# Optimization experiments

Measured on AMD Instinct MI355X. Metric: run time of the kernel, lower is better.

The kernel has to match this reference:

```python
import jax, jax.numpy as jnp
import numpy as np
from jax import lax

CLASSES = 6
R = 8            # zoom_factor
FEAT = 32        # DUC loops i,j in range(32)
OUT_PAD = 304    # DUC hardcodes zeros(b,6,304,304)
IMG = 256        # original image H=W -> final bilinear resize target
BN_EPS = 1e-5
DN = ('NCHW', 'OIHW', 'NCHW')


def _duc(x):
    # x: [B, classes*r*r, H', W'] ; original loop only reads top-left 32x32
    x = x[:, :, :FEAT, :FEAT]
    B = x.shape[0]
    # channel order in original: view(b, classes, r*r) -> (classes, r, r)
    y = x.reshape(B, CLASSES, R, R, FEAT, FEAT)
    y = y.transpose(0, 1, 4, 2, 5, 3).reshape(B, CLASSES, FEAT * R, FEAT * R)  # [B,6,256,256]
    pad = OUT_PAD - FEAT * R
    return jnp.pad(y, ((0, 0), (0, 0), (0, pad), (0, pad)))  # zeros ring like torch.zeros buffer


def _bilinear_align_corners(x, oh, ow):
    b, c, h, w = x.shape
    ys = jnp.linspace(0.0, h - 1.0, oh)
    xs = jnp.linspace(0.0, w - 1.0, ow)
    y0 = jnp.floor(ys).astype(jnp.int32)
    x0 = jnp.floor(xs).astype(jnp.int32)
    y1 = jnp.minimum(y0 + 1, h - 1)
    x1 = jnp.minimum(x0 + 1, w - 1)
    wy = (ys - y0)[None, None, :, None]
    wx = (xs - x0)[None, None, None, :]
    rows = x[:, :, y0, :] * (1.0 - wy) + x[:, :, y1, :] * wy          # [b,c,oh,w]
    out = rows[:, :, :, x0] * (1.0 - wx) + rows[:, :, :, x1] * wx     # [b,c,oh,ow]
    return out


def setup_inputs() -> dict:
    key = jax.random.key(0)
    ks = jax.random.split(key, 8)
    x = jax.random.normal(ks[0], (16, 5632, 32, 32), jnp.float32)
    w1 = jax.random.normal(ks[1], (512, 5632, 1, 1), jnp.float32) * 0.02
    gamma = 1.0 + 0.1 * jax.random.normal(ks[2], (512,), jnp.float32)
    beta = 0.1 * jax.random.normal(ks[3], (512,), jnp.float32)
    mean = 0.1 * jax.random.normal(ks[4], (512,), jnp.float32)
    var = jax.random.uniform(ks[5], (512,), jnp.float32, 0.5, 1.5)
    w2 = jax.random.normal(ks[6], (CLASSES * R * R, 512, 1, 1), jnp.float32) * 0.02
    b2 = jax.random.normal(ks[7], (CLASSES * R * R,), jnp.float32) * 0.02
    return {'x': x, 'w1': w1, 'gamma': gamma, 'beta': beta, 'mean': mean, 'var': var, 'w2': w2, 'b2': b2}


def reference(x, w1, gamma, beta, mean, var, w2, b2):
    # cls head: 1x1 conv with padding=1 (quirk in source) -> 34x34 map
    h = lax.conv_general_dilated(x, w1, (1, 1), ((1, 1), (1, 1)), dimension_numbers=DN)
    inv = lax.rsqrt(var + BN_EPS)
    h = (h - mean[None, :, None, None]) * (inv * gamma)[None, :, None, None] + beta[None, :, None, None]
    h = jax.nn.relu(h)  # Dropout2d is identity at inference
    h = lax.conv_general_dilated(h, w2, (1, 1), ((0, 0), (0, 0)), dimension_numbers=DN)
    h = h + b2[None, :, None, None]            # [B,384,34,34]
    h = _duc(h)                                # [B,6,304,304]
    h = jax.nn.softmax(h, axis=1)
    return _bilinear_align_corners(h, IMG, IMG)  # [B,6,256,256]
```

## Files before the change

### kernel.cpp

```cpp
#include <hip/hip_runtime.h>
#include <hip/hip_bf16.h>
#include <stdint.h>

typedef float f32x4 __attribute__((ext_vector_type(4)));
typedef short s16x8 __attribute__((ext_vector_type(8)));
typedef unsigned short u16;

__device__ __forceinline__ u16 f2bf(float f) {
  uint32_t u = __float_as_uint(f);
  u = (u + 0x7fffu + ((u >> 16) & 1u)) >> 16;
  return (u16)u;
}

__device__ __forceinline__ u16 cvt_bf(float f) {
  union { __hip_bfloat16 h; u16 u; } c;
  c.h = __float2bfloat16(f);
  return c.u;
}

__device__ __forceinline__ void wg_barrier_lds() {
  __builtin_amdgcn_sched_barrier(0);
  asm volatile("s_waitcnt lgkmcnt(0)" ::: "memory");
  __builtin_amdgcn_s_barrier();
  __builtin_amdgcn_sched_barrier(0);
}

__global__ void k_params(const float* __restrict__ gamma, const float* __restrict__ beta,
                         const float* __restrict__ mean, const float* __restrict__ var,
                         float* __restrict__ bnS, float* __restrict__ bnT) {
  int i = threadIdx.x;
  if (i < 512) {
    float s = gamma[i] * rsqrtf(var[i] + 1e-5f);
    bnS[i] = s;
    bnT[i] = beta[i] - mean[i] * s;
  }
}

__global__ void k_convert(const float* __restrict__ in, u16* __restrict__ out, int n4) {
  int i = blockIdx.x * blockDim.x + threadIdx.x;
  if (i < n4) {
    float4 v = ((const float4*)in)[i];
    ushort4 o;
    o.x = f2bf(v.x); o.y = f2bf(v.y); o.z = f2bf(v.z); o.w = f2bf(v.w);
    ((ushort4*)out)[i] = o;
  }
}

__global__ void k_border2(const float* __restrict__ w2, const float* __restrict__ b2,
                          const float* __restrict__ bnT, float* __restrict__ border2) {
  int o = blockIdx.x;
  int l = threadIdx.x;
  float s = 0.f;
  for (int j = 0; j < 8; ++j) {
    int c = l + 64 * j;
    s += w2[o * 512 + c] * fmaxf(bnT[c], 0.f);
  }
  for (int off = 32; off > 0; off >>= 1) s += __shfl_down(s, off, 64);
  if (l == 0) border2[o] = s + b2[o];
}

__global__ __launch_bounds__(256, 2) void k_gemm1(
    const float* __restrict__ X, const u16* __restrict__ Bw,
    const float* __restrict__ bnS, const float* __restrict__ bnT,
    u16* __restrict__ H) {
  const int K = 5632;
  const int NT = 176;
  __shared__ __align__(16) u16 sA[2][128 * 40];
  __shared__ __align__(16) u16 sB[2][4096];
  int nb = gridDim.x;
  int id = blockIdx.x;
  int li = (id & 7) * (nb >> 3) + (id >> 3);
  int nt = li & 3;
  int mt = li >> 2;
  int t = threadIdx.x;
  int l = t & 63, w = t >> 6;
  int wm = w >> 1, wn = w & 1;

  auto swz = [](int u) { int m = u >> 2, g = u & 3; return (m * 4 + (g ^ ((m >> 1) & 3))) * 8; };
  int wo0 = swz(t), wo1 = swz(t + 256);
  const u16* gB0 = Bw + (size_t)(nt * 128 + (t >> 2)) * K + (t & 3) * 8;
  const u16* gB1 = gB0 + (size_t)64 * K;

  int m0 = (w >> 1) * 64 + 2 * (l & 31);
  int kh = w & 1, kq = l >> 5;
  int bidx = mt >> 3, p0 = (mt & 7) * 128;
  const float* gA = X + (size_t)bidx * (5632ull * 1024) + (size_t)(kh * 16 + kq * 8) * 1024
                      + p0 + m0;
  int aoff = m0 * 40 + kh * 16 + kq * 8;

  int offA[4], offB[4];
#pragma unroll
  for (int f = 0; f < 4; ++f) {
    int m = wm * 64 + f * 16 + (l & 15);
    offA[f] = m * 40 + (l >> 4) * 8;
    int n = wn * 64 + f * 16 + (l & 15);
    int g = l >> 4;
    offB[f] = (n * 4 + (g ^ ((n >> 1) & 3))) * 8;
  }

  f32x4 acc[4][4] = {};

  auto loadA = [&](float2* va) {
#pragma unroll
    for (int ii = 0; ii < 8; ++ii) va[ii] = *(const float2*)(gA + (size_t)ii * 1024);
  };
  auto stage = [&](const float2* va, s16x8 r0, s16x8 r1, u16* bA, u16* bB) {
    union { u16 u[16]; s16x8 v[2]; } cv;
#pragma unroll
    for (int ii = 0; ii < 8; ++ii) {
      cv.u[ii] = cvt_bf(va[ii].x);
      cv.u[8 + ii] = cvt_bf(va[ii].y);
    }
    *(s16x8*)(bA + aoff) = cv.v[0];
    *(s16x8*)(bA + aoff + 40) = cv.v[1];
    *(s16x8*)(bB + wo0) = r0;
    *(s16x8*)(bB + wo1) = r1;
  };
  auto compute = [&](const u16* bA, const u16* bB) {
    s16x8 af[4], bfr[4];
#pragma unroll
    for (int f = 0; f < 4; ++f) {
      af[f] = *(const s16x8*)(bA + offA[f]);
      bfr[f] = *(const s16x8*)(bB + offB[f]);
    }
#pragma unroll
    for (int ii = 0; ii < 4; ++ii)
#pragma unroll
      for (int j = 0; j < 4; ++j)
        acc[ii][j] = __builtin_amdgcn_mfma_f32_16x16x32_bf16(af[ii], bfr[j], acc[ii][j], 0, 0, 0);
  };

  float2 vaA[8], vaB[8];
  s16x8 rBa0, rBa1, rBb0, rBb1;

  loadA(vaA); rBa0 = *(const s16x8*)gB0; rBa1 = *(const s16x8*)gB1;
  stage(vaA, rBa0, rBa1, sA[0], sB[0]);
  gA += 32 * 1024; gB0 += 32; gB1 += 32;
  loadA(vaB); rBb0 = *(const s16x8*)gB0; rBb1 = *(const s16x8*)gB1;

  for (int i = 0; i < NT; i += 2) {
    wg_barrier_lds();
    if (i + 2 < NT) {
      gA += 32 * 1024; gB0 += 32; gB1 += 32;
      loadA(vaA); rBa0 = *(const s16x8*)gB0; rBa1 = *(const s16x8*)gB1;
    }
    compute(sA[0], sB[0]);
    stage(vaB, rBb0, rBb1, sA[1], sB[1]);
    wg_barrier_lds();
    if (i + 3 < NT) {
      gA += 32 * 1024; gB0 += 32; gB1 += 32;
      loadA(vaB); rBb0 = *(const s16x8*)gB0; rBb1 = *(const s16x8*)gB1;
    }
    compute(sA[1], sB[1]);
    if (i + 2 < NT) stage(vaA, rBa0, rBa1, sA[0], sB[0]);
  }

  int mb = mt * 128 + wm * 64;
  int nbase = nt * 128 + wn * 64;
#pragma unroll
  for (int j = 0; j < 4; ++j) {
    int n_g = nbase + j * 16 + (l & 15);
    float s = bnS[n_g], tt = bnT[n_g];
#pragma unroll
    for (int i = 0; i < 4; ++i)
#pragma unroll
      for (int r = 0; r < 4; ++r) {
        int m_g = mb + i * 16 + (l >> 4) * 4 + r;
        float v = fmaxf(acc[i][j][r] * s + tt, 0.f);
        H[(size_t)m_g * 512 + n_g] = f2bf(v);
      }
  }
}

__global__ __launch_bounds__(256, 2) void k_gemm2(
    const u16* __restrict__ A, const u16* __restrict__ B,
    const float* __restrict__ b2, float* __restrict__ C) {
  const int K = 512;
  __shared__ __align__(16) u16 sA[4096];
  __shared__ __align__(16) u16 sB[4096];
  int nb = gridDim.x;
  int id = blockIdx.x;
  int li = (id & 7) * (nb >> 3) + (id >> 3);
  int nt = li % 3;
  int mt = li / 3;
  int t = threadIdx.x;
  int l = t & 63, w = t >> 6;
  int wm = w >> 1, wn = w & 1;

  auto swz = [](int u) { int m = u >> 2, g = u & 3; return (m * 4 + (g ^ ((m >> 1) & 3))) * 8; };
  int wo0 = swz(t), wo1 = swz(t + 256);

  const u16* gA0 = A + (size_t)(mt * 128 + (t >> 2)) * K + (t & 3) * 8;
  const u16* gA1 = gA0 + (size_t)64 * K;
  const u16* gB0 = B + (size_t)(nt * 128 + (t >> 2)) * K + (t & 3) * 8;
  const u16* gB1 = gB0 + (size_t)64 * K;

  int offA[4], offB[4];
#pragma unroll
  for (int f = 0; f < 4; ++f) {
    int g = l >> 4;
    int m = wm * 64 + f * 16 + (l & 15);
    offA[f] = (m * 4 + (g ^ ((m >> 1) & 3))) * 8;
    int n = wn * 64 + f * 16 + (l & 15);
    offB[f] = (n * 4 + (g ^ ((n >> 1) & 3))) * 8;
  }

  f32x4 acc[4][4] = {};

  s16x8 rA0 = *(const s16x8*)gA0;
  s16x8 rA1 = *(const s16x8*)gA1;
  s16x8 rB0 = *(const s16x8*)gB0;
  s16x8 rB1 = *(const s16x8*)gB1;

  for (int k0 = 0; k0 < K; k0 += 32) {
    *(s16x8*)(sA + wo0) = rA0;
    *(s16x8*)(sA + wo1) = rA1;
    *(s16x8*)(sB + wo0) = rB0;
    *(s16x8*)(sB + wo1) = rB1;
    wg_barrier_lds();
    if (k0 + 32 < K) {
      gA0 += 32; gA1 += 32; gB0 += 32; gB1 += 32;
      rA0 = *(const s16x8*)gA0;
      rA1 = *(const s16x8*)gA1;
      rB0 = *(const s16x8*)gB0;
      rB1 = *(const s16x8*)gB1;
    }
    s16x8 af[4], bf[4];
#pragma unroll
    for (int f = 0; f < 4; ++f) {
      af[f] = *(const s16x8*)(sA + offA[f]);
      bf[f] = *(const s16x8*)(sB + offB[f]);
    }
#pragma unroll
    for (int i = 0; i < 4; ++i)
#pragma unroll
      for (int j = 0; j < 4; ++j)
        acc[i][j] = __builtin_amdgcn_mfma_f32_16x16x32_bf16(af[i], bf[j], acc[i][j], 0, 0, 0);
    wg_barrier_lds();
  }

  int mb = mt * 128 + wm * 64;
  int nbase = nt * 128 + wn * 64;
#pragma unroll
  for (int j = 0; j < 4; ++j) {
    int n_g = nbase + j * 16 + (l & 15);
    float bias = b2[n_g];
#pragma unroll
    for (int i = 0; i < 4; ++i)
#pragma unroll
      for (int r = 0; r < 4; ++r) {
        int m_g = mb + i * 16 + (l >> 4) * 4 + r;
        C[(size_t)m_g * 384 + n_g] = acc[i][j][r] + bias;
      }
  }
}

__global__ __launch_bounds__(256) void k_out(const float* __restrict__ c2,
                                             const float* __restrict__ border2,
                                             float* __restrict__ out) {
  int b = blockIdx.x >> 8;
  int oy = blockIdx.x & 255;
  int ox = threadIdx.x;
  const float SCL = 303.0f / 255.0f;
  float ys = oy * SCL, xs = ox * SCL;
  int y0 = (int)ys; if (y0 > 303) y0 = 303;
  int x0 = (int)xs; if (x0 > 303) x0 = 303;
  float wy = ys - (float)y0, wx = xs - (float)x0;
  int y1 = y0 + 1; if (y1 > 303) y1 = 303;
  int x1 = x0 + 1; if (x1 > 303) x1 = 303;
  int syA[2] = {y0, y1};
  int sxA[2] = {x0, x1};
  float wyA[2] = {1.f - wy, wy};
  float wxA[2] = {1.f - wx, wx};
  float acc[6] = {0.f, 0.f, 0.f, 0.f, 0.f, 0.f};
#pragma unroll
  for (int cy = 0; cy < 2; ++cy) {
#pragma unroll
    for (int cx = 0; cx < 2; ++cx) {
      float wgt = wyA[cy] * wxA[cx];
      int sy = syA[cy], sx = sxA[cx];
      if (sy >= 256 || sx >= 256) {
        float p = wgt * (1.f / 6.f);
#pragma unroll
        for (int c = 0; c < 6; ++c) acc[c] += p;
      } else {
        int i = sy >> 3, j = sx >> 3;
        int sub = ((sy & 7) << 3) | (sx & 7);
        const float* src;
        if (i == 0 || j == 0)
          src = border2 + sub;
        else
          src = c2 + (size_t)((b << 10) + ((i - 1) << 5) + (j - 1)) * 384 + sub;
        float l0 = src[0],   l1 = src[64],  l2 = src[128];
        float l3 = src[192], l4 = src[256], l5 = src[320];
        float mx = fmaxf(fmaxf(fmaxf(l0, l1), fmaxf(l2, l3)), fmaxf(l4, l5));
        float e0 = __expf(l0 - mx), e1 = __expf(l1 - mx), e2 = __expf(l2 - mx);
        float e3 = __expf(l3 - mx), e4 = __expf(l4 - mx), e5 = __expf(l5 - mx);
        float ssum = e0 + e1 + e2 + e3 + e4 + e5;
        float r = wgt / ssum;
        acc[0] += e0 * r; acc[1] += e1 * r; acc[2] += e2 * r;
        acc[3] += e3 * r; acc[4] += e4 * r; acc[5] += e5 * r;
      }
    }
  }
  size_t base = ((size_t)b * 6) << 16;
  int pix = (oy << 8) | ox;
#pragma unroll
  for (int c = 0; c < 6; ++c) out[base + ((size_t)c << 16) + pix] = acc[c];
}

extern "C" void kernel_launch(void* const* d_in, const int* in_sizes, int n_in,
                              void* d_out, int out_size, void* d_ws, size_t ws_size,
                              hipStream_t stream) {
  const float* x     = (const float*)d_in[0];
  const float* w1    = (const float*)d_in[1];
  const float* gamma = (const float*)d_in[2];
  const float* beta  = (const float*)d_in[3];
  const float* mean  = (const float*)d_in[4];
  const float* var   = (const float*)d_in[5];
  const float* w2    = (const float*)d_in[6];
  const float* b2    = (const float*)d_in[7];
  float* out = (float*)d_out;

  char* ws = (char*)d_ws;
  size_t off = 0;
  auto alloc = [&](size_t bytes) -> char* {
    char* p = ws + off;
    off = (off + bytes + 255) & ~(size_t)255;
    return p;
  };
  u16*   w1bf    = (u16*)alloc(512ull * 5632 * 2);
  u16*   w2bf    = (u16*)alloc(384ull * 512 * 2);
  float* bnS     = (float*)alloc(512 * 4);
  float* bnT     = (float*)alloc(512 * 4);
  float* border2 = (float*)alloc(384 * 4);
  u16*   h       = (u16*)alloc(16384ull * 512 * 2);
  float* c2      = (float*)alloc(16384ull * 384 * 4);
  (void)ws_size;

  k_params<<<dim3(1), dim3(512), 0, stream>>>(gamma, beta, mean, var, bnS, bnT);
  k_convert<<<dim3(2816), dim3(256), 0, stream>>>(w1, w1bf, 512 * 5632 / 4);
  k_convert<<<dim3(192), dim3(256), 0, stream>>>(w2, w2bf, 384 * 512 / 4);
  k_border2<<<dim3(384), dim3(64), 0, stream>>>(w2, b2, bnT, border2);

  k_gemm1<<<dim3(512), dim3(256), 0, stream>>>(x, w1bf, bnS, bnT, h);
  k_gemm2<<<dim3(128 * 3), dim3(256), 0, stream>>>(h, w2bf, b2, c2);
  k_out<<<dim3(16 * 256), dim3(256), 0, stream>>>(c2, border2, out);
}
```

Measured before the change: 259.1 us.

## Split-K the first GEMM into two halves with a combine kernel

GEMM1 is split along K into two halves, launching 1024 blocks instead of 512. Each block writes fp32 partial sums to a workspace buffer, and a new combine kernel adds the halves and applies BN, ReLU and the bf16 conversion. The goal is to fill the device better than 512 blocks do, since at 2 blocks per CU they may not cover all CUs. In exchange it writes and reads two 32 MB fp32 partial buffers and adds a launch. It falls back to the old path when the workspace is too small.

Result: slower. 264.7 us (+2.2%).

```diff
diff --git a/kernel.cpp b/kernel.cpp
--- a/kernel.cpp
+++ b/kernel.cpp
@@ -59,17 +59,20 @@
   if (l == 0) border2[o] = s + b2[o];
 }
 
+template <int MODE>
 __global__ __launch_bounds__(256, 2) void k_gemm1(
     const float* __restrict__ X, const u16* __restrict__ Bw,
     const float* __restrict__ bnS, const float* __restrict__ bnT,
-    u16* __restrict__ H) {
+    u16* __restrict__ H, float* __restrict__ P) {
   const int K = 5632;
-  const int NT = 176;
+  const int NT = (MODE == 1) ? 88 : 176;
   __shared__ __align__(16) u16 sA[2][128 * 40];
   __shared__ __align__(16) u16 sB[2][4096];
-  int nb = gridDim.x;
   int id = blockIdx.x;
-  int li = (id & 7) * (nb >> 3) + (id >> 3);
+  int inner = id & 511;
+  int kh = (MODE == 1) ? (id >> 9) : 0;
+  int kbase = kh * 2816;
+  int li = (inner & 7) * 64 + (inner >> 3);
   int nt = li & 3;
   int mt = li >> 2;
   int t = threadIdx.x;
@@ -78,15 +81,15 @@
 
   auto swz = [](int u) { int m = u >> 2, g = u & 3; return (m * 4 + (g ^ ((m >> 1) & 3))) * 8; };
   int wo0 = swz(t), wo1 = swz(t + 256);
-  const u16* gB0 = Bw + (size_t)(nt * 128 + (t >> 2)) * K + (t & 3) * 8;
+  const u16* gB0 = Bw + (size_t)(nt * 128 + (t >> 2)) * K + kbase + (t & 3) * 8;
   const u16* gB1 = gB0 + (size_t)64 * K;
 
   int m0 = (w >> 1) * 64 + 2 * (l & 31);
-  int kh = w & 1, kq = l >> 5;
+  int kh2 = w & 1, kq = l >> 5;
   int bidx = mt >> 3, p0 = (mt & 7) * 128;
-  const float* gA = X + (size_t)bidx * (5632ull * 1024) + (size_t)(kh * 16 + kq * 8) * 1024
-                      + p0 + m0;
-  int aoff = m0 * 40 + kh * 16 + kq * 8;
+  const float* gA = X + (size_t)bidx * (5632ull * 1024)
+                      + (size_t)(kbase + kh2 * 16 + kq * 8) * 1024 + p0 + m0;
+  int aoff = m0 * 40 + kh2 * 16 + kq * 8;
 
   int offA[4], offB[4];
 #pragma unroll
@@ -157,19 +160,51 @@
 
   int mb = mt * 128 + wm * 64;
   int nbase = nt * 128 + wn * 64;
-#pragma unroll
-  for (int j = 0; j < 4; ++j) {
-    int n_g = nbase + j * 16 + (l & 15);
-    float s = bnS[n_g], tt = bnT[n_g];
-#pragma unroll
-    for (int i = 0; i < 4; ++i)
-#pragma unroll
-      for (int r = 0; r < 4; ++r) {
-        int m_g = mb + i * 16 + (l >> 4) * 4 + r;
-        float v = fmaxf(acc[i][j][r] * s + tt, 0.f);
-        H[(size_t)m_g * 512 + n_g] = f2bf(v);
-      }
-  }
+  if (MODE == 0) {
+#pragma unroll
+    for (int j = 0; j < 4; ++j) {
+      int n_g = nbase + j * 16 + (l & 15);
+      float s = bnS[n_g], tt = bnT[n_g];
+#pragma unroll
+      for (int i = 0; i < 4; ++i)
+#pragma unroll
+        for (int r = 0; r < 4; ++r) {
+          int m_g = mb + i * 16 + (l >> 4) * 4 + r;
+          float v = fmaxf(acc[i][j][r] * s + tt, 0.f);
+          H[(size_t)m_g * 512 + n_g] = f2bf(v);
+        }
+    }
+  } else {
+    float* Pd = P + (size_t)kh * (16384ull * 512);
+#pragma unroll
+    for (int j = 0; j < 4; ++j) {
+      int n_g = nbase + j * 16 + (l & 15);
+#pragma unroll
+      for (int i = 0; i < 4; ++i)
+#pragma unroll
+        for (int r = 0; r < 4; ++r) {
+          int m_g = mb + i * 16 + (l >> 4) * 4 + r;
+          Pd[(size_t)m_g * 512 + n_g] = acc[i][j][r];
+        }
+    }
+  }
+}
+
+__global__ __launch_bounds__(256) void k_combine(
+    const float* __restrict__ P, const float* __restrict__ bnS,
+    const float* __restrict__ bnT, u16* __restrict__ H) {
+  int i = blockIdx.x * 256 + threadIdx.x;
+  const float4 a = ((const float4*)P)[i];
+  const float4 b = ((const float4*)(P + 16384ull * 512))[i];
+  int n0 = (i * 4) & 511;
+  float4 s = *(const float4*)(bnS + n0);
+  float4 tt = *(const float4*)(bnT + n0);
+  ushort4 o;
+  o.x = cvt_bf(fmaxf((a.x + b.x) * s.x + tt.x, 0.f));
+  o.y = cvt_bf(fmaxf((a.y + b.y) * s.y + tt.y, 0.f));
+  o.z = cvt_bf(fmaxf((a.z + b.z) * s.z + tt.z, 0.f));
+  o.w = cvt_bf(fmaxf((a.w + b.w) * s.w + tt.w, 0.f));
+  ((ushort4*)H)[i] = o;
 }
 
 __global__ __launch_bounds__(256, 2) void k_gemm2(
@@ -336,14 +371,22 @@
   float* border2 = (float*)alloc(384 * 4);
   u16*   h       = (u16*)alloc(16384ull * 512 * 2);
   float* c2      = (float*)alloc(16384ull * 384 * 4);
-  (void)ws_size;
+
+  const size_t PB = 16384ull * 512 * 4;
+  bool split = (off + 2 * PB + 4096 <= ws_size);
+  float* P = split ? (float*)alloc(2 * PB) : nullptr;
 
   k_params<<<dim3(1), dim3(512), 0, stream>>>(gamma, beta, mean, var, bnS, bnT);
   k_convert<<<dim3(2816), dim3(256), 0, stream>>>(w1, w1bf, 512 * 5632 / 4);
   k_convert<<<dim3(192), dim3(256), 0, stream>>>(w2, w2bf, 384 * 512 / 4);
   k_border2<<<dim3(384), dim3(64), 0, stream>>>(w2, b2, bnT, border2);
 
-  k_gemm1<<<dim3(512), dim3(256), 0, stream>>>(x, w1bf, bnS, bnT, h);
+  if (split) {
+    k_gemm1<1><<<dim3(1024), dim3(256), 0, stream>>>(x, w1bf, bnS, bnT, h, P);
+    k_combine<<<dim3(8192), dim3(256), 0, stream>>>(P, bnS, bnT, h);
+  } else {
+    k_gemm1<0><<<dim3(512), dim3(256), 0, stream>>>(x, w1bf, bnS, bnT, h, nullptr);
+  }
   k_gemm2<<<dim3(128 * 3), dim3(256), 0, stream>>>(h, w2bf, b2, c2);
   k_out<<<dim3(16 * 256), dim3(256), 0, stream>>>(c2, border2, out);
 }
```
